# Performance work log

Hardware: AMD Instinct MI355X
Metric: run time of the kernel (lower is better)

The kernel has to match this reference:

```python
import jax, jax.numpy as jnp
import numpy as np

N = 65536        # nodes = x_feature_num * batch_size
F_IN = 1024      # x_feature_num (conv1 in_channels)
E = 2097152      # edges (avg degree 32)
B = 64           # batch_size (final Linear out_features)


def gcn_conv(x, src, dst, ew, W, b, n):
    """PyG GCNConv: linear -> sym-normalized scatter-add with self-loops (fill=1)."""
    h = x @ W                                              # [n, out]
    deg = jnp.zeros((n,), x.dtype).at[dst].add(ew) + 1.0   # in-degree incl. self-loop weight 1
    dinv = jax.lax.rsqrt(deg)                              # deg >= 1, no inf
    norm = dinv[src] * ew * dinv[dst]                      # [E]
    agg = jnp.zeros_like(h).at[dst].add(h[src] * norm[:, None])
    agg = agg + h * (dinv * dinv)[:, None]                 # self-loop messages
    return agg + b


def setup_inputs() -> dict:
    key = jax.random.key(0)
    ks = jax.random.split(key, 12)
    x = jax.random.normal(ks[0], (N, F_IN), dtype=jnp.float32)
    A = jax.random.randint(ks[1], (2, E), 0, N, dtype=jnp.int32)
    A_weights = jax.random.uniform(ks[2], (E,), dtype=jnp.float32)
    s = 0.05
    W1 = jax.random.normal(ks[3], (F_IN, 16), dtype=jnp.float32) * s
    b1 = jnp.zeros((16,), jnp.float32)
    W2 = jax.random.normal(ks[4], (16, 4), dtype=jnp.float32) * s
    b2 = jnp.zeros((4,), jnp.float32)
    W3 = jax.random.normal(ks[5], (4, 1), dtype=jnp.float32) * s
    b3 = jnp.zeros((1,), jnp.float32)
    W_out = jax.random.normal(ks[6], (B, N), dtype=jnp.float32) * (1.0 / np.sqrt(N))
    b_out = jnp.zeros((B,), jnp.float32)
    return {"x": x, "A": A, "A_weights": A_weights,
            "W1": W1, "b1": b1, "W2": W2, "b2": b2, "W3": W3, "b3": b3,
            "W_out": W_out, "b_out": b_out}


def reference(x, A, A_weights, W1, b1, W2, b2, W3, b3, W_out, b_out):
    src, dst = A[0], A[1]
    n = x.shape[0]
    h = jax.nn.relu(gcn_conv(x, src, dst, A_weights, W1, b1, n))
    # F.dropout is identity in eval mode
    h = jax.nn.relu(gcn_conv(h, src, dst, A_weights, W2, b2, n))
    h = jax.nn.relu(gcn_conv(h, src, dst, A_weights, W3, b3, n))
    flat = h.reshape(-1)                                   # [N]
    return flat @ W_out.T + b_out                          # [B]
```

## Files before the change

### kernel.cpp

```cpp
#include <hip/hip_runtime.h>

#define NNODES 65536
#define FIN 1024
#define NEDGES 2097152
#define NB 64
#define G 256
#define CH (NEDGES / G)
#define CAPR 96
#define CAPB 9216
#define SCAP 10240
#define XRG 772
#define XSR 12
#define WRG 132

__global__ __launch_bounds__(256) void kgemmF(const float* __restrict__ x, const float* __restrict__ W1,
                                              float* __restrict__ h1) {
  __shared__ float sx[8 * XRG];
  __shared__ float sw[8 * WRG];
  const int t = threadIdx.x;
  const int jg2 = t & 1, ks = (t >> 1) & 7, rg = t >> 4;
  const int row0 = blockIdx.x * 64;
  float4 accA[4], accB[4];
#pragma unroll
  for (int ri = 0; ri < 4; ++ri) {
    accA[ri] = make_float4(0.f, 0.f, 0.f, 0.f);
    accB[ri] = make_float4(0.f, 0.f, 0.f, 0.f);
  }
  for (int ch = 0; ch < 16; ++ch) {
    const int c0 = ch * 64;
#pragma unroll
    for (int i = 0; i < 4; ++i) {
      const int v = t + i * 256;
      const int rr = v >> 4, kq = v & 15;
      *(float4*)&sx[(kq >> 1) * XRG + rr * XSR + (kq & 1) * 4] =
          *(const float4*)(x + (size_t)(row0 + rr) * FIN + c0 + kq * 4);
    }
    {
      const int kr = t >> 2, c4 = t & 3;
      *(float4*)&sw[(kr >> 3) * WRG + (kr & 7) * 16 + c4 * 4] =
          *(const float4*)(W1 + (size_t)(c0 + kr) * 16 + c4 * 4);
    }
    __syncthreads();
    const int xb = ks * XRG + rg * (4 * XSR);
    const int wb = ks * WRG + jg2 * 8;
#pragma unroll
    for (int k4 = 0; k4 < 2; ++k4) {
      float4 x4[4];
#pragma unroll
      for (int ri = 0; ri < 4; ++ri) x4[ri] = *(const float4*)&sx[xb + ri * XSR + k4 * 4];
#pragma unroll
      for (int kqi = 0; kqi < 4; ++kqi) {
        const float4 wa = *(const float4*)&sw[wb + (k4 * 4 + kqi) * 16];
        const float4 wbv = *(const float4*)&sw[wb + (k4 * 4 + kqi) * 16 + 4];
        const float xs0 = (kqi == 0) ? x4[0].x : (kqi == 1) ? x4[0].y : (kqi == 2) ? x4[0].z : x4[0].w;
        const float xs1 = (kqi == 0) ? x4[1].x : (kqi == 1) ? x4[1].y : (kqi == 2) ? x4[1].z : x4[1].w;
        const float xs2 = (kqi == 0) ? x4[2].x : (kqi == 1) ? x4[2].y : (kqi == 2) ? x4[2].z : x4[2].w;
        const float xs3 = (kqi == 0) ? x4[3].x : (kqi == 1) ? x4[3].y : (kqi == 2) ? x4[3].z : x4[3].w;
        accA[0].x = fmaf(xs0, wa.x, accA[0].x); accA[0].y = fmaf(xs0, wa.y, accA[0].y);
        accA[0].z = fmaf(xs0, wa.z, accA[0].z); accA[0].w = fmaf(xs0, wa.w, accA[0].w);
        accB[0].x = fmaf(xs0, wbv.x, accB[0].x); accB[0].y = fmaf(xs0, wbv.y, accB[0].y);
        accB[0].z = fmaf(xs0, wbv.z, accB[0].z); accB[0].w = fmaf(xs0, wbv.w, accB[0].w);
        accA[1].x = fmaf(xs1, wa.x, accA[1].x); accA[1].y = fmaf(xs1, wa.y, accA[1].y);
        accA[1].z = fmaf(xs1, wa.z, accA[1].z); accA[1].w = fmaf(xs1, wa.w, accA[1].w);
        accB[1].x = fmaf(xs1, wbv.x, accB[1].x); accB[1].y = fmaf(xs1, wbv.y, accB[1].y);
        accB[1].z = fmaf(xs1, wbv.z, accB[1].z); accB[1].w = fmaf(xs1, wbv.w, accB[1].w);
        accA[2].x = fmaf(xs2, wa.x, accA[2].x); accA[2].y = fmaf(xs2, wa.y, accA[2].y);
        accA[2].z = fmaf(xs2, wa.z, accA[2].z); accA[2].w = fmaf(xs2, wa.w, accA[2].w);
        accB[2].x = fmaf(xs2, wbv.x, accB[2].x); accB[2].y = fmaf(xs2, wbv.y, accB[2].y);
        accB[2].z = fmaf(xs2, wbv.z, accB[2].z); accB[2].w = fmaf(xs2, wbv.w, accB[2].w);
        accA[3].x = fmaf(xs3, wa.x, accA[3].x); accA[3].y = fmaf(xs3, wa.y, accA[3].y);
        accA[3].z = fmaf(xs3, wa.z, accA[3].z); accA[3].w = fmaf(xs3, wa.w, accA[3].w);
        accB[3].x = fmaf(xs3, wbv.x, accB[3].x); accB[3].y = fmaf(xs3, wbv.y, accB[3].y);
        accB[3].z = fmaf(xs3, wbv.z, accB[3].z); accB[3].w = fmaf(xs3, wbv.w, accB[3].w);
      }
    }
    __syncthreads();
  }
#pragma unroll
  for (int off = 2; off <= 8; off <<= 1) {
#pragma unroll
    for (int ri = 0; ri < 4; ++ri) {
      accA[ri].x += __shfl_xor(accA[ri].x, off, 64);
      accA[ri].y += __shfl_xor(accA[ri].y, off, 64);
      accA[ri].z += __shfl_xor(accA[ri].z, off, 64);
      accA[ri].w += __shfl_xor(accA[ri].w, off, 64);
      accB[ri].x += __shfl_xor(accB[ri].x, off, 64);
      accB[ri].y += __shfl_xor(accB[ri].y, off, 64);
      accB[ri].z += __shfl_xor(accB[ri].z, off, 64);
      accB[ri].w += __shfl_xor(accB[ri].w, off, 64);
    }
  }
  if (ks == 0) {
#pragma unroll
    for (int ri = 0; ri < 4; ++ri) {
      float* hp = h1 + (size_t)(row0 + rg * 4 + ri) * 16 + jg2 * 8;
      *(float4*)hp = accA[ri];
      *(float4*)(hp + 4) = accB[ri];
    }
  }
}

__global__ __launch_bounds__(512) void kscatF(const int* __restrict__ src, const int* __restrict__ dst,
                                              const float* __restrict__ ew, int2* __restrict__ tmp,
                                              int* __restrict__ counts) {
  __shared__ int2 ent[CH];
  __shared__ int hist[256], excl[256], cursor[256], sh[256];
  const int t = threadIdx.x, blk = blockIdx.x;
  const int base = blk * CH;
  if (t < 256) hist[t] = 0;
  __syncthreads();
  int sa[16], da[16]; float wa[16];
#pragma unroll
  for (int i = 0; i < 16; ++i) {
    const int e = base + t + i * 512;
    sa[i] = src[e]; da[i] = dst[e]; wa[i] = ew[e];
    atomicAdd(&hist[((unsigned)da[i]) >> 8], 1);
  }
  __syncthreads();
  if (t < 256) sh[t] = hist[t];
  __syncthreads();
#pragma unroll
  for (int off = 1; off < 256; off <<= 1) {
    int a = (t < 256 && t >= off) ? sh[t - off] : 0;
    __syncthreads();
    if (t < 256) sh[t] += a;
    __syncthreads();
  }
  if (t < 256) {
    const int e = sh[t] - hist[t];
    excl[t] = e;
    cursor[t] = e;
    counts[t * 256 + blk] = hist[t];
  }
  __syncthreads();
#pragma unroll
  for (int i = 0; i < 16; ++i) {
    const int b = ((unsigned)da[i]) >> 8;
    const int pos = atomicAdd(&cursor[b], 1);
    ent[pos] = make_int2((sa[i] & 0xFFFF) | ((da[i] & 255) << 16) | (b << 24),
                         __float_as_int(wa[i]));
  }
  __syncthreads();
#pragma unroll
  for (int i = 0; i < 16; ++i) {
    const int idx = t + i * 512;
    const int2 p = ent[idx];
    const int b = ((unsigned)p.x) >> 24;
    const int local = idx - excl[b];
    if (local < CAPR)
      tmp[(size_t)(b * 256 + blk) * CAPR + local] = make_int2(p.x & 0x00FFFFFF, p.y);
  }
}

__global__ __launch_bounds__(1024) void ksortE(const int2* __restrict__ tmp, const int* __restrict__ counts,
                                               int2* __restrict__ csr, int* __restrict__ rs,
                                               int* __restrict__ cnt, float* __restrict__ dinv,
                                               float* __restrict__ h1) {
  __shared__ int2 stg[SCAP];
  __shared__ int hist[256], excl[256], cursor[256];
  __shared__ float degacc[256], dloc[256];
  const int t = threadIdx.x, b = blockIdx.x;
  const int seg = t >> 2, q4 = t & 3;
  const int len = counts[b * 256 + seg];
  const size_t cellbase = (size_t)(b * 256 + seg) * CAPR;
  if (t < 256) { hist[t] = 0; degacc[t] = 0.f; }
  __syncthreads();
  for (int i = q4; i < len; i += 4) {
    const int2 p = tmp[cellbase + i];
    const int fine = (p.x >> 16) & 255;
    atomicAdd(&hist[fine], 1);
    atomicAdd(&degacc[fine], __int_as_float(p.y));
  }
  __syncthreads();
  if (t < 256) excl[t] = hist[t];
  __syncthreads();
#pragma unroll
  for (int off = 1; off < 256; off <<= 1) {
    int a = (t < 256 && t >= off) ? excl[t - off] : 0;
    __syncthreads();
    if (t < 256) excl[t] += a;
    __syncthreads();
  }
  if (t < 256) {
    const int e = excl[t] - hist[t];
    cursor[t] = e;
    rs[b * 256 + t] = b * CAPB + e;
    cnt[b * 256 + t] = hist[t];
    const float dn = rsqrtf(1.0f + degacc[t]);
    dloc[t] = dn;
    dinv[b * 256 + t] = dn;
  }
  __syncthreads();
  for (int i = q4; i < len; i += 4) {
    const int2 p = tmp[cellbase + i];
    const int fine = (p.x >> 16) & 255;
    const int pos = atomicAdd(&cursor[fine], 1);
    const int2 rec = make_int2(p.x & 0xFFFF, p.y);
    if (pos < SCAP) stg[pos] = rec;
    else csr[(size_t)b * CAPB + pos] = rec;
  }
  __syncthreads();
  const int ntot = excl[255];
  for (int j = t; j < ntot; j += 1024) csr[(size_t)b * CAPB + j] = stg[j];
  {
    const int node = t >> 2, q = t & 3;
    float* hp = h1 + (size_t)(b * 256 + node) * 16 + q * 4;
    float4 h = *(float4*)hp;
    const float dn = dloc[node];
    h.x *= dn; h.y *= dn; h.z *= dn; h.w *= dn;
    *(float4*)hp = h;
  }
}

__global__ __launch_bounds__(256) void kgather1(const float* __restrict__ H1, const int* __restrict__ rs,
                                                const int* __restrict__ cnt, const int2* __restrict__ csr,
                                                const float* __restrict__ dinv,
                                                const float* __restrict__ W2, const float* __restrict__ b1,
                                                float* __restrict__ H2) {
  __shared__ float sh_t[4][16];
  const int tid = threadIdx.x, wv = tid >> 6, l = tid & 63;
  const int n = blockIdx.x * 4 + wv;
  const int f4 = l & 3, slot = l >> 2;
  const int beg = rs[n], len = cnt[n];
  float4 acc = make_float4(0.f, 0.f, 0.f, 0.f);
  int2 pcur;
  if (slot < len) pcur = csr[beg + slot];
  for (int j = slot; j < len; j += 16) {
    const int jn = j + 16;
    int2 pnext;
    if (jn < len) pnext = csr[beg + jn];
    const float w = __int_as_float(pcur.y);
    const float4 hv = *(const float4*)(H1 + (size_t)pcur.x * 16 + f4 * 4);
    acc.x = fmaf(w, hv.x, acc.x);
    acc.y = fmaf(w, hv.y, acc.y);
    acc.z = fmaf(w, hv.z, acc.z);
    acc.w = fmaf(w, hv.w, acc.w);
    pcur = pnext;
  }
#pragma unroll
  for (int off = 4; off < 64; off <<= 1) {
    acc.x += __shfl_xor(acc.x, off, 64);
    acc.y += __shfl_xor(acc.y, off, 64);
    acc.z += __shfl_xor(acc.z, off, 64);
    acc.w += __shfl_xor(acc.w, off, 64);
  }
  if (slot == 0) {
    const float dn = dinv[n];
    const float4 hs = *(const float4*)(H1 + (size_t)n * 16 + f4 * 4);
    float t0 = dn * (acc.x + hs.x) + b1[f4 * 4 + 0];
    float t1 = dn * (acc.y + hs.y) + b1[f4 * 4 + 1];
    float t2 = dn * (acc.z + hs.z) + b1[f4 * 4 + 2];
    float t3 = dn * (acc.w + hs.w) + b1[f4 * 4 + 3];
    sh_t[wv][f4 * 4 + 0] = t0 > 0.f ? t0 : 0.f;
    sh_t[wv][f4 * 4 + 1] = t1 > 0.f ? t1 : 0.f;
    sh_t[wv][f4 * 4 + 2] = t2 > 0.f ? t2 : 0.f;
    sh_t[wv][f4 * 4 + 3] = t3 > 0.f ? t3 : 0.f;
  }
  __syncthreads();
  if (tid < 16) {
    const int w2 = tid >> 2, c = tid & 3;
    const int nn = blockIdx.x * 4 + w2;
    float s = 0.f;
#pragma unroll
    for (int ff = 0; ff < 16; ++ff) s = fmaf(sh_t[w2][ff], W2[ff * 4 + c], s);
    H2[(size_t)nn * 4 + c] = s * dinv[nn];
  }
}

__global__ __launch_bounds__(256) void kgather2(const float* __restrict__ H2, const int* __restrict__ rs,
                                                const int* __restrict__ cnt, const int2* __restrict__ csr,
                                                const float* __restrict__ dinv,
                                                const float* __restrict__ W3, const float* __restrict__ b2,
                                                float* __restrict__ H3) {
  const int tid = threadIdx.x, wv = tid >> 6, l = tid & 63;
  const int n = blockIdx.x * 4 + wv;
  const int f = l & 3, slot = l >> 2;
  const int beg = rs[n], len = cnt[n];
  float acc = 0.f;
  for (int j = slot; j < len; j += 16) {
    const int2 p = csr[beg + j];
    acc = fmaf(__int_as_float(p.y), H2[(size_t)p.x * 4 + f], acc);
  }
#pragma unroll
  for (int off = 4; off < 64; off <<= 1) acc += __shfl_xor(acc, off, 64);
  const float dn = dinv[n];
  float t = dn * (acc + H2[(size_t)n * 4 + f]) + b2[f];
  t = t > 0.f ? t : 0.f;
  float p = t * W3[f];
  p += __shfl_xor(p, 1, 64);
  p += __shfl_xor(p, 2, 64);
  if (l == 0) H3[n] = p * dn;
}

__global__ __launch_bounds__(256) void kgather3(const float* __restrict__ H3, const int* __restrict__ rs,
                                                const int* __restrict__ cnt, const int2* __restrict__ csr,
                                                const float* __restrict__ dinv,
                                                const float* __restrict__ b3, float* __restrict__ flat,
                                                const float* __restrict__ bout, float* __restrict__ out) {
  const int tid = threadIdx.x, wv = tid >> 6, l = tid & 63;
  if (blockIdx.x == 0 && tid < NB) out[tid] = bout[tid];
  const int n = blockIdx.x * 4 + wv;
  const int beg = rs[n], len = cnt[n];
  float acc = 0.f;
  for (int j = l; j < len; j += 64) {
    const int2 p = csr[beg + j];
    acc = fmaf(__int_as_float(p.y), H3[p.x], acc);
  }
#pragma unroll
  for (int off = 1; off < 64; off <<= 1) acc += __shfl_xor(acc, off, 64);
  if (l == 0) {
    const float dn = dinv[n];
    float t = dn * (acc + H3[n]) + b3[0];
    flat[n] = t > 0.f ? t : 0.f;
  }
}

__global__ __launch_bounds__(256) void kfinal(const float* __restrict__ flat, const float* __restrict__ Wout,
                                              float* __restrict__ out) {
  const int b = blockIdx.x >> 4, q = blockIdx.x & 15;
  const float4* __restrict__ f4 = (const float4*)(flat) + q * 1024;
  const float4* __restrict__ w4 = (const float4*)(Wout + (size_t)b * NNODES) + q * 1024;
  __shared__ float red[4];
  float s = 0.f;
  for (int i = threadIdx.x; i < 1024; i += 256) {
    const float4 a = f4[i];
    const float4 wv = w4[i];
    s += a.x * wv.x + a.y * wv.y + a.z * wv.z + a.w * wv.w;
  }
#pragma unroll
  for (int off = 32; off; off >>= 1) s += __shfl_down(s, off, 64);
  if ((threadIdx.x & 63) == 0) red[threadIdx.x >> 6] = s;
  __syncthreads();
  if (threadIdx.x == 0) atomicAdd(&out[b], red[0] + red[1] + red[2] + red[3]);
}

extern "C" void kernel_launch(void* const* d_in, const int* in_sizes, int n_in,
                              void* d_out, int out_size, void* d_ws, size_t ws_size,
                              hipStream_t stream) {
  const float* x   = (const float*)d_in[0];
  const int*   A   = (const int*)d_in[1];
  const float* ew  = (const float*)d_in[2];
  const float* W1  = (const float*)d_in[3];
  const float* b1  = (const float*)d_in[4];
  const float* W2  = (const float*)d_in[5];
  const float* b2  = (const float*)d_in[6];
  const float* W3  = (const float*)d_in[7];
  const float* b3  = (const float*)d_in[8];
  const float* Wo  = (const float*)d_in[9];
  const float* bo  = (const float*)d_in[10];
  float* out = (float*)d_out;

  const int* src = A;
  const int* dst = A + NEDGES;

  char* p = (char*)d_ws;
  float* dinv   = (float*)p; p += sizeof(float) * NNODES;
  int*   rsofs  = (int*)p;   p += sizeof(int) * NNODES;
  int*   cnt    = (int*)p;   p += sizeof(int) * NNODES;
  int*   counts = (int*)p;   p += sizeof(int) * NNODES;
  int2*  tmp    = (int2*)p;  p += sizeof(int2) * (size_t)NNODES * CAPR;
  int2*  csr    = (int2*)p;  p += sizeof(int2) * (size_t)G * CAPB;
  float* h1     = (float*)p; p += sizeof(float) * (size_t)NNODES * 16;
  float* H2     = (float*)p; p += sizeof(float) * (size_t)NNODES * 4;
  float* H3     = (float*)p; p += sizeof(float) * NNODES;
  float* flat   = (float*)p; p += sizeof(float) * NNODES;

  kgemmF<<<NNODES / 64, 256, 0, stream>>>(x, W1, h1);
  kscatF<<<G, 512, 0, stream>>>(src, dst, ew, tmp, counts);
  ksortE<<<G, 1024, 0, stream>>>(tmp, counts, csr, rsofs, cnt, dinv, h1);
  kgather1<<<NNODES / 4, 256, 0, stream>>>(h1, rsofs, cnt, csr, dinv, W2, b1, H2);
  kgather2<<<NNODES / 4, 256, 0, stream>>>(H2, rsofs, cnt, csr, dinv, W3, b2, H3);
  kgather3<<<NNODES / 4, 256, 0, stream>>>(H3, rsofs, cnt, csr, dinv, b3, flat, bo, out);
  kfinal<<<NB * 16, 256, 0, stream>>>(flat, Wo, out);
}
```

Measured before the change: 195.3 us.

## Fuse edge bucketing scatter and first GEMM into one heterogeneous launch

Merges the edge coarse-bucketing kernel and the x@W1 GEMM into one launch whose first 512 blocks do the edge scatter and whose remaining blocks do the GEMM, sharing shared memory through a union. The scatter now uses 512 blocks of 256 threads with a smaller per-cell capacity of 48, and the sort kernel reads 512 segments per bucket with 2 threads each. The aim is to overlap the memory-bound GEMM with the scatter and drop one launch. The trade-offs are a larger shared-memory footprint on the GEMM blocks, which may lower occupancy, and the tighter per-cell cap, which could overflow on skewed degree distributions.

```diff
diff --git a/kernel.cpp b/kernel.cpp
--- a/kernel.cpp
+++ b/kernel.cpp
@@ -5,150 +5,153 @@
 #define NEDGES 2097152
 #define NB 64
 #define G 256
-#define CH (NEDGES / G)
-#define CAPR 96
+#define SCATB 512
+#define CH2 (NEDGES / SCATB)
+#define CAPR 48
 #define CAPB 9216
 #define SCAP 10240
 #define XRG 772
 #define XSR 12
 #define WRG 132
 
-__global__ __launch_bounds__(256) void kgemmF(const float* __restrict__ x, const float* __restrict__ W1,
-                                              float* __restrict__ h1) {
-  __shared__ float sx[8 * XRG];
-  __shared__ float sw[8 * WRG];
+union ASMem {
+  struct { float sx[8 * XRG]; float sw[8 * WRG]; } g;
+  struct { int2 ent[CH2]; int hist[256], excl[256], cursor[256], sh[256]; } s;
+};
+
+__global__ __launch_bounds__(256) void kfusedA(const float* __restrict__ x, const float* __restrict__ W1,
+                                               float* __restrict__ h1, const int* __restrict__ src,
+                                               const int* __restrict__ dst, const float* __restrict__ ew,
+                                               int2* __restrict__ tmp, int* __restrict__ counts) {
+  __shared__ ASMem sm;
   const int t = threadIdx.x;
-  const int jg2 = t & 1, ks = (t >> 1) & 7, rg = t >> 4;
-  const int row0 = blockIdx.x * 64;
-  float4 accA[4], accB[4];
-#pragma unroll
-  for (int ri = 0; ri < 4; ++ri) {
-    accA[ri] = make_float4(0.f, 0.f, 0.f, 0.f);
-    accB[ri] = make_float4(0.f, 0.f, 0.f, 0.f);
-  }
-  for (int ch = 0; ch < 16; ++ch) {
-    const int c0 = ch * 64;
-#pragma unroll
-    for (int i = 0; i < 4; ++i) {
-      const int v = t + i * 256;
-      const int rr = v >> 4, kq = v & 15;
-      *(float4*)&sx[(kq >> 1) * XRG + rr * XSR + (kq & 1) * 4] =
-          *(const float4*)(x + (size_t)(row0 + rr) * FIN + c0 + kq * 4);
+  if (blockIdx.x < SCATB) {
+    const int blk = blockIdx.x;
+    const int base = blk * CH2;
+    sm.s.hist[t] = 0;
+    __syncthreads();
+    int sa[16], da[16]; float wa[16];
+#pragma unroll
+    for (int i = 0; i < 16; ++i) {
+      const int e = base + t + i * 256;
+      sa[i] = src[e]; da[i] = dst[e]; wa[i] = ew[e];
+      atomicAdd(&sm.s.hist[((unsigned)da[i]) >> 8], 1);
+    }
+    __syncthreads();
+    sm.s.sh[t] = sm.s.hist[t];
+    __syncthreads();
+#pragma unroll
+    for (int off = 1; off < 256; off <<= 1) {
+      int a = (t >= off) ? sm.s.sh[t - off] : 0;
+      __syncthreads();
+      sm.s.sh[t] += a;
+      __syncthreads();
     }
     {
-      const int kr = t >> 2, c4 = t & 3;
-      *(float4*)&sw[(kr >> 3) * WRG + (kr & 7) * 16 + c4 * 4] =
-          *(const float4*)(W1 + (size_t)(c0 + kr) * 16 + c4 * 4);
-    }
-    __syncthreads();
-    const int xb = ks * XRG + rg * (4 * XSR);
-    const int wb = ks * WRG + jg2 * 8;
-#pragma unroll
-    for (int k4 = 0; k4 < 2; ++k4) {
-      float4 x4[4];
-#pragma unroll
-      for (int ri = 0; ri < 4; ++ri) x4[ri] = *(const float4*)&sx[xb + ri * XSR + k4 * 4];
-#pragma unroll
-      for (int kqi = 0; kqi < 4; ++kqi) {
-        const float4 wa = *(const float4*)&sw[wb + (k4 * 4 + kqi) * 16];
-        const float4 wbv = *(const float4*)&sw[wb + (k4 * 4 + kqi) * 16 + 4];
-        const float xs0 = (kqi == 0) ? x4[0].x : (kqi == 1) ? x4[0].y : (kqi == 2) ? x4[0].z : x4[0].w;
-        const float xs1 = (kqi == 0) ? x4[1].x : (kqi == 1) ? x4[1].y : (kqi == 2) ? x4[1].z : x4[1].w;
-        const float xs2 = (kqi == 0) ? x4[2].x : (kqi == 1) ? x4[2].y : (kqi == 2) ? x4[2].z : x4[2].w;
-        const float xs3 = (kqi == 0) ? x4[3].x : (kqi == 1) ? x4[3].y : (kqi == 2) ? x4[3].z : x4[3].w;
-        accA[0].x = fmaf(xs0, wa.x, accA[0].x); accA[0].y = fmaf(xs0, wa.y, accA[0].y);
-        accA[0].z = fmaf(xs0, wa.z, accA[0].z); accA[0].w = fmaf(xs0, wa.w, accA[0].w);
-        accB[0].x = fmaf(xs0, wbv.x, accB[0].x); accB[0].y = fmaf(xs0, wbv.y, accB[0].y);
-        accB[0].z = fmaf(xs0, wbv.z, accB[0].z); accB[0].w = fmaf(xs0, wbv.w, accB[0].w);
-        accA[1].x = fmaf(xs1, wa.x, accA[1].x); accA[1].y = fmaf(xs1, wa.y, accA[1].y);
-        accA[1].z = fmaf(xs1, wa.z, accA[1].z); accA[1].w = fmaf(xs1, wa.w, accA[1].w);
-        accB[1].x = fmaf(xs1, wbv.x, accB[1].x); accB[1].y = fmaf(xs1, wbv.y, accB[1].y);
-        accB[1].z = fmaf(xs1, wbv.z, accB[1].z); accB[1].w = fmaf(xs1, wbv.w, accB[1].w);
-        accA[2].x = fmaf(xs2, wa.x, accA[2].x); accA[2].y = fmaf(xs2, wa.y, accA[2].y);
-        accA[2].z = fmaf(xs2, wa.z, accA[2].z); accA[2].w = fmaf(xs2, wa.w, accA[2].w);
-        accB[2].x = fmaf(xs2, wbv.x, accB[2].x); accB[2].y = fmaf(xs2, wbv.y, accB[2].y);
-        accB[2].z = fmaf(xs2, wbv.z, accB[2].z); accB[2].w = fmaf(xs2, wbv.w, accB[2].w);
-        accA[3].x = fmaf(xs3, wa.x, accA[3].x); accA[3].y = fmaf(xs3, wa.y, accA[3].y);
-        accA[3].z = fmaf(xs3, wa.z, accA[3].z); accA[3].w = fmaf(xs3, wa.w, accA[3].w);
-        accB[3].x = fmaf(xs3, wbv.x, accB[3].x); accB[3].y = fmaf(xs3, wbv.y, accB[3].y);
-        accB[3].z = fmaf(xs3, wbv.z, accB[3].z); accB[3].w = fmaf(xs3, wbv.w, accB[3].w);
-      }
-    }
-    __syncthreads();
-  }
-#pragma unroll
-  for (int off = 2; off <= 8; off <<= 1) {
+      const int e = sm.s.sh[t] - sm.s.hist[t];
+      sm.s.excl[t] = e;
+      sm.s.cursor[t] = e;
+      counts[t * SCATB + blk] = sm.s.hist[t];
+    }
+    __syncthreads();
+#pragma unroll
+    for (int i = 0; i < 16; ++i) {
+      const int b = ((unsigned)da[i]) >> 8;
+      const int pos = atomicAdd(&sm.s.cursor[b], 1);
+      sm.s.ent[pos] = make_int2((sa[i] & 0xFFFF) | ((da[i] & 255) << 16) | (b << 24),
+                                __float_as_int(wa[i]));
+    }
+    __syncthreads();
+#pragma unroll
+    for (int i = 0; i < 16; ++i) {
+      const int idx = t + i * 256;
+      const int2 p = sm.s.ent[idx];
+      const int b = ((unsigned)p.x) >> 24;
+      const int local = idx - sm.s.excl[b];
+      if (local < CAPR)
+        tmp[(size_t)(b * SCATB + blk) * CAPR + local] = make_int2(p.x & 0x00FFFFFF, p.y);
+    }
+  } else {
+    const int jg2 = t & 1, ks = (t >> 1) & 7, rg = t >> 4;
+    const int row0 = (blockIdx.x - SCATB) * 64;
+    float4 accA[4], accB[4];
 #pragma unroll
     for (int ri = 0; ri < 4; ++ri) {
-      accA[ri].x += __shfl_xor(accA[ri].x, off, 64);
-      accA[ri].y += __shfl_xor(accA[ri].y, off, 64);
-      accA[ri].z += __shfl_xor(accA[ri].z, off, 64);
-      accA[ri].w += __shfl_xor(accA[ri].w, off, 64);
-      accB[ri].x += __shfl_xor(accB[ri].x, off, 64);
-      accB[ri].y += __shfl_xor(accB[ri].y, off, 64);
-      accB[ri].z += __shfl_xor(accB[ri].z, off, 64);
-      accB[ri].w += __shfl_xor(accB[ri].w, off, 64);
-    }
-  }
-  if (ks == 0) {
-#pragma unroll
-    for (int ri = 0; ri < 4; ++ri) {
-      float* hp = h1 + (size_t)(row0 + rg * 4 + ri) * 16 + jg2 * 8;
-      *(float4*)hp = accA[ri];
-      *(float4*)(hp + 4) = accB[ri];
-    }
-  }
-}
-
-__global__ __launch_bounds__(512) void kscatF(const int* __restrict__ src, const int* __restrict__ dst,
-                                              const float* __restrict__ ew, int2* __restrict__ tmp,
-                                              int* __restrict__ counts) {
-  __shared__ int2 ent[CH];
-  __shared__ int hist[256], excl[256], cursor[256], sh[256];
-  const int t = threadIdx.x, blk = blockIdx.x;
-  const int base = blk * CH;
-  if (t < 256) hist[t] = 0;
-  __syncthreads();
-  int sa[16], da[16]; float wa[16];
-#pragma unroll
-  for (int i = 0; i < 16; ++i) {
-    const int e = base + t + i * 512;
-    sa[i] = src[e]; da[i] = dst[e]; wa[i] = ew[e];
-    atomicAdd(&hist[((unsigned)da[i]) >> 8], 1);
-  }
-  __syncthreads();
-  if (t < 256) sh[t] = hist[t];
-  __syncthreads();
-#pragma unroll
-  for (int off = 1; off < 256; off <<= 1) {
-    int a = (t < 256 && t >= off) ? sh[t - off] : 0;
-    __syncthreads();
-    if (t < 256) sh[t] += a;
-    __syncthreads();
-  }
-  if (t < 256) {
-    const int e = sh[t] - hist[t];
-    excl[t] = e;
-    cursor[t] = e;
-    counts[t * 256 + blk] = hist[t];
-  }
-  __syncthreads();
-#pragma unroll
-  for (int i = 0; i < 16; ++i) {
-    const int b = ((unsigned)da[i]) >> 8;
-    const int pos = atomicAdd(&cursor[b], 1);
-    ent[pos] = make_int2((sa[i] & 0xFFFF) | ((da[i] & 255) << 16) | (b << 24),
-                         __float_as_int(wa[i]));
-  }
-  __syncthreads();
-#pragma unroll
-  for (int i = 0; i < 16; ++i) {
-    const int idx = t + i * 512;
-    const int2 p = ent[idx];
-    const int b = ((unsigned)p.x) >> 24;
-    const int local = idx - excl[b];
-    if (local < CAPR)
-      tmp[(size_t)(b * 256 + blk) * CAPR + local] = make_int2(p.x & 0x00FFFFFF, p.y);
+      accA[ri] = make_float4(0.f, 0.f, 0.f, 0.f);
+      accB[ri] = make_float4(0.f, 0.f, 0.f, 0.f);
+    }
+    for (int ch = 0; ch < 16; ++ch) {
+      const int c0 = ch * 64;
+#pragma unroll
+      for (int i = 0; i < 4; ++i) {
+        const int v = t + i * 256;
+        const int rr = v >> 4, kq = v & 15;
+        *(float4*)&sm.g.sx[(kq >> 1) * XRG + rr * XSR + (kq & 1) * 4] =
+            *(const float4*)(x + (size_t)(row0 + rr) * FIN + c0 + kq * 4);
+      }
+      {
+        const int kr = t >> 2, c4 = t & 3;
+        *(float4*)&sm.g.sw[(kr >> 3) * WRG + (kr & 7) * 16 + c4 * 4] =
+            *(const float4*)(W1 + (size_t)(c0 + kr) * 16 + c4 * 4);
+      }
+      __syncthreads();
+      const int xb = ks * XRG + rg * (4 * XSR);
+      const int wb = ks * WRG + jg2 * 8;
+#pragma unroll
+      for (int k4 = 0; k4 < 2; ++k4) {
+        float4 x4[4];
+#pragma unroll
+        for (int ri = 0; ri < 4; ++ri) x4[ri] = *(const float4*)&sm.g.sx[xb + ri * XSR + k4 * 4];
+#pragma unroll
+        for (int kqi = 0; kqi < 4; ++kqi) {
+          const float4 wa = *(const float4*)&sm.g.sw[wb + (k4 * 4 + kqi) * 16];
+          const float4 wbv = *(const float4*)&sm.g.sw[wb + (k4 * 4 + kqi) * 16 + 4];
+          const float xs0 = (kqi == 0) ? x4[0].x : (kqi == 1) ? x4[0].y : (kqi == 2) ? x4[0].z : x4[0].w;
+          const float xs1 = (kqi == 0) ? x4[1].x : (kqi == 1) ? x4[1].y : (kqi == 2) ? x4[1].z : x4[1].w;
+          const float xs2 = (kqi == 0) ? x4[2].x : (kqi == 1) ? x4[2].y : (kqi == 2) ? x4[2].z : x4[2].w;
+          const float xs3 = (kqi == 0) ? x4[3].x : (kqi == 1) ? x4[3].y : (kqi == 2) ? x4[3].z : x4[3].w;
+          accA[0].x = fmaf(xs0, wa.x, accA[0].x); accA[0].y = fmaf(xs0, wa.y, accA[0].y);
+          accA[0].z = fmaf(xs0, wa.z, accA[0].z); accA[0].w = fmaf(xs0, wa.w, accA[0].w);
+          accB[0].x = fmaf(xs0, wbv.x, accB[0].x); accB[0].y = fmaf(xs0, wbv.y, accB[0].y);
+          accB[0].z = fmaf(xs0, wbv.z, accB[0].z); accB[0].w = fmaf(xs0, wbv.w, accB[0].w);
+          accA[1].x = fmaf(xs1, wa.x, accA[1].x); accA[1].y = fmaf(xs1, wa.y, accA[1].y);
+          accA[1].z = fmaf(xs1, wa.z, accA[1].z); accA[1].w = fmaf(xs1, wa.w, accA[1].w);
+          accB[1].x = fmaf(xs1, wbv.x, accB[1].x); accB[1].y = fmaf(xs1, wbv.y, accB[1].y);
+          accB[1].z = fmaf(xs1, wbv.z, accB[1].z); accB[1].w = fmaf(xs1, wbv.w, accB[1].w);
+          accA[2].x = fmaf(xs2, wa.x, accA[2].x); accA[2].y = fmaf(xs2, wa.y, accA[2].y);
+          accA[2].z = fmaf(xs2, wa.z, accA[2].z); accA[2].w = fmaf(xs2, wa.w, accA[2].w);
+          accB[2].x = fmaf(xs2, wbv.x, accB[2].x); accB[2].y = fmaf(xs2, wbv.y, accB[2].y);
+          accB[2].z = fmaf(xs2, wbv.z, accB[2].z); accB[2].w = fmaf(xs2, wbv.w, accB[2].w);
+          accA[3].x = fmaf(xs3, wa.x, accA[3].x); accA[3].y = fmaf(xs3, wa.y, accA[3].y);
+          accA[3].z = fmaf(xs3, wa.z, accA[3].z); accA[3].w = fmaf(xs3, wa.w, accA[3].w);
+          accB[3].x = fmaf(xs3, wbv.x, accB[3].x); accB[3].y = fmaf(xs3, wbv.y, accB[3].y);
+          accB[3].z = fmaf(xs3, wbv.z, accB[3].z); accB[3].w = fmaf(xs3, wbv.w, accB[3].w);
+        }
+      }
+      __syncthreads();
+    }
+#pragma unroll
+    for (int off = 2; off <= 8; off <<= 1) {
+#pragma unroll
+      for (int ri = 0; ri < 4; ++ri) {
+        accA[ri].x += __shfl_xor(accA[ri].x, off, 64);
+        accA[ri].y += __shfl_xor(accA[ri].y, off, 64);
+        accA[ri].z += __shfl_xor(accA[ri].z, off, 64);
+        accA[ri].w += __shfl_xor(accA[ri].w, off, 64);
+        accB[ri].x += __shfl_xor(accB[ri].x, off, 64);
+        accB[ri].y += __shfl_xor(accB[ri].y, off, 64);
+        accB[ri].z += __shfl_xor(accB[ri].z, off, 64);
+        accB[ri].w += __shfl_xor(accB[ri].w, off, 64);
+      }
+    }
+    if (ks == 0) {
+#pragma unroll
+      for (int ri = 0; ri < 4; ++ri) {
+        float* hp = h1 + (size_t)(row0 + rg * 4 + ri) * 16 + jg2 * 8;
+        *(float4*)hp = accA[ri];
+        *(float4*)(hp + 4) = accB[ri];
+      }
+    }
   }
 }
 
@@ -160,12 +163,12 @@
   __shared__ int hist[256], excl[256], cursor[256];
   __shared__ float degacc[256], dloc[256];
   const int t = threadIdx.x, b = blockIdx.x;
-  const int seg = t >> 2, q4 = t & 3;
-  const int len = counts[b * 256 + seg];
-  const size_t cellbase = (size_t)(b * 256 + seg) * CAPR;
+  const int seg = t >> 1, q2 = t & 1;
+  const int len = counts[b * SCATB + seg];
+  const size_t cellbase = (size_t)(b * SCATB + seg) * CAPR;
   if (t < 256) { hist[t] = 0; degacc[t] = 0.f; }
   __syncthreads();
-  for (int i = q4; i < len; i += 4) {
+  for (int i = q2; i < len; i += 2) {
     const int2 p = tmp[cellbase + i];
     const int fine = (p.x >> 16) & 255;
     atomicAdd(&hist[fine], 1);
@@ -191,7 +194,7 @@
     dinv[b * 256 + t] = dn;
   }
   __syncthreads();
-  for (int i = q4; i < len; i += 4) {
+  for (int i = q2; i < len; i += 2) {
     const int2 p = tmp[cellbase + i];
     const int fine = (p.x >> 16) & 255;
     const int pos = atomicAdd(&cursor[fine], 1);
@@ -357,16 +360,15 @@
   float* dinv   = (float*)p; p += sizeof(float) * NNODES;
   int*   rsofs  = (int*)p;   p += sizeof(int) * NNODES;
   int*   cnt    = (int*)p;   p += sizeof(int) * NNODES;
-  int*   counts = (int*)p;   p += sizeof(int) * NNODES;
-  int2*  tmp    = (int2*)p;  p += sizeof(int2) * (size_t)NNODES * CAPR;
+  int*   counts = (int*)p;   p += sizeof(int) * G * SCATB;
+  int2*  tmp    = (int2*)p;  p += sizeof(int2) * (size_t)G * SCATB * CAPR;
   int2*  csr    = (int2*)p;  p += sizeof(int2) * (size_t)G * CAPB;
   float* h1     = (float*)p; p += sizeof(float) * (size_t)NNODES * 16;
   float* H2     = (float*)p; p += sizeof(float) * (size_t)NNODES * 4;
   float* H3     = (float*)p; p += sizeof(float) * NNODES;
   float* flat   = (float*)p; p += sizeof(float) * NNODES;
 
-  kgemmF<<<NNODES / 64, 256, 0, stream>>>(x, W1, h1);
-  kscatF<<<G, 512, 0, stream>>>(src, dst, ew, tmp, counts);
+  kfusedA<<<SCATB + NNODES / 64, 256, 0, stream>>>(x, W1, h1, src, dst, ew, tmp, counts);
   ksortE<<<G, 1024, 0, stream>>>(tmp, counts, csr, rsofs, cnt, dinv, h1);
   kgather1<<<NNODES / 4, 256, 0, stream>>>(h1, rsofs, cnt, csr, dinv, W2, b1, H2);
   kgather2<<<NNODES / 4, 256, 0, stream>>>(H2, rsofs, cnt, csr, dinv, W3, b2, H3);
```

Measured after the change: 191.1 us. -2.1%, faster.
